# Performance work log

Measured on AMD Instinct MI355X. Metric: run time of the kernel, lower is better.

The kernel has to match this reference:

```python
import jax, jax.numpy as jnp
import numpy as np

SEQ_LEN = 4096
N_FEAT = 2048
N_PADD = 128


def setup_inputs() -> dict:
    key = jax.random.key(0)
    kx, kw = jax.random.split(key)
    x = jax.random.normal(kx, (SEQ_LEN, N_FEAT), dtype=jnp.float32)
    # Fused QKV dense: features = 3 * n_feat
    W = jax.random.normal(kw, (N_FEAT, 3 * N_FEAT), dtype=jnp.float32) * (1.0 / np.sqrt(N_FEAT))
    b = jnp.zeros((3 * N_FEAT,), dtype=jnp.float32)
    return {"x": x, "W": W, "b": b, "n_padd": N_PADD}


def reference(x, W, b, n_padd):
    # Fused QKV projection, split along feature axis (as in nn.Dense + jnp.split)
    qkv = x @ W + b  # [S, 3F]
    q, k, v = jnp.split(qkv, 3, axis=1)  # each [S, F]
    S, F = q.shape
    idx = jnp.arange(S)
    # scores[i, j] = q_i . k_j / sqrt(F)
    scores = (q @ k.T) * (1.0 / jnp.sqrt(jnp.float32(F)))  # [S, S]
    seq_mask = idx >= n_padd                      # valid (non-padding) positions
    causal = idx[None, :] <= idx[:, None]         # j <= i
    mask = causal & seq_mask[None, :]             # kernel: causal_mask & seq_mask
    row_valid = seq_mask                          # rows < n_padd are not computed/stored
    neg_inf = jnp.float32(-jnp.inf)
    scores = jnp.where(mask, scores, neg_inf)
    # Fully-masked (padding) rows would softmax to NaN; neutralize then zero output.
    scores = jnp.where(row_valid[:, None], scores, 0.0)
    att = jax.nn.softmax(scores, axis=-1)         # row-wise stable softmax
    out = att @ v                                 # [S, F]
    out = jnp.where(row_valid[:, None], out, 0.0)  # padded rows produce zeros
    return out
```

## Files before the change

kernel.cpp:

```cpp
#include <hip/hip_runtime.h>
#include <cstdint>
#include <cstddef>
#include <cmath>

typedef unsigned short u16;
typedef short v8s __attribute__((ext_vector_type(8)));
typedef float v4f __attribute__((ext_vector_type(4)));

constexpr int SEQ = 4096;
constexpr int FEAT = 2048;
constexpr int F3 = 6144;


__device__ __forceinline__ u16 f2bf(float f) {
  union { float f; uint32_t u; } v; v.f = f;
  uint32_t r = v.u + 0x7FFFu + ((v.u >> 16) & 1u);
  return (u16)(r >> 16);
}

__device__ __forceinline__ float bf2f(u16 s) {
  union { uint32_t u; float f; } v; v.u = ((uint32_t)s) << 16;
  return v.f;
}

__device__ __forceinline__ void gld_lds16(const u16* g, u16* l) {
  __builtin_amdgcn_global_load_lds(
      (const __attribute__((address_space(1))) void*)g,
      (__attribute__((address_space(3))) void*)l, 16, 0, 0);
}


__global__ void cvt_f32_bf16(const float* __restrict__ in, u16* __restrict__ out, int n8) {
  int i = blockIdx.x * 256 + threadIdx.x;
  if (i >= n8) return;
  const float4* p = (const float4*)in + (size_t)i * 2;
  float4 a = p[0], b = p[1];
  union { u16 s[8]; uint4 v; } u;
  u.s[0] = f2bf(a.x); u.s[1] = f2bf(a.y); u.s[2] = f2bf(a.z); u.s[3] = f2bf(a.w);
  u.s[4] = f2bf(b.x); u.s[5] = f2bf(b.y); u.s[6] = f2bf(b.z); u.s[7] = f2bf(b.w);
  *(uint4*)(out + (size_t)i * 8) = u.v;
}

__global__ void transp_f2b(const float* __restrict__ in, int ldin,
                           u16* __restrict__ out, int ldout) {
  __shared__ float tile[32][33];
  int c0 = blockIdx.x * 32, r0 = blockIdx.y * 32;
  int tx = threadIdx.x, ty = threadIdx.y;
#pragma unroll
  for (int p = 0; p < 4; ++p)
    tile[ty + 8 * p][tx] = in[(size_t)(r0 + ty + 8 * p) * ldin + c0 + tx];
  __syncthreads();
#pragma unroll
  for (int p = 0; p < 4; ++p)
    out[(size_t)(c0 + ty + 8 * p) * ldout + r0 + tx] = f2bf(tile[tx][ty + 8 * p]);
}

__global__ void transp_b2b(const u16* __restrict__ in, int ldin,
                           u16* __restrict__ out, int ldout) {
  __shared__ u16 tile[32][33];
  int c0 = blockIdx.x * 32, r0 = blockIdx.y * 32;
  int tx = threadIdx.x, ty = threadIdx.y;
#pragma unroll
  for (int p = 0; p < 4; ++p)
    tile[ty + 8 * p][tx] = in[(size_t)(r0 + ty + 8 * p) * ldin + c0 + tx];
  __syncthreads();
#pragma unroll
  for (int p = 0; p < 4; ++p)
    out[(size_t)(c0 + ty + 8 * p) * ldout + r0 + tx] = tile[tx][ty + 8 * p];
}


#define BARW() asm volatile("s_barrier" ::: "memory")
#define VMC6() asm volatile("s_waitcnt vmcnt(6)" ::: "memory")

#define STAGE(SB, KO) do { \
  u16* Lb = &LDSU[SB][0] + w * 512; \
  gld_lds16(pA0 + (KO), Lb); \
  gld_lds16(pA0 + (size_t)64 * LDA_ + (KO), Lb + 2048); \
  gld_lds16(pB0 + (KO), Lb + 4096); \
  gld_lds16(pB0 + (size_t)64 * LDB_ + (KO), Lb + 4096 + 2048); \
  gld_lds16(pB0 + (size_t)128 * LDB_ + (KO), Lb + 4096 + 4096); \
  gld_lds16(pB0 + (size_t)192 * LDB_ + (KO), Lb + 4096 + 6144); \
} while (0)

#define LOADA(BUF) do { _Pragma("unroll") \
  for (int mi = 0; mi < 8; ++mi) \
    af[mi] = *(const v8s*)(&LDSU[BUF][0] + (mi * 16 + lm) * 32 + lqs); \
} while (0)

#define LOADB(BUF) do { _Pragma("unroll") \
  for (int ni = 0; ni < 4; ++ni) \
    bf4[ni] = *(const v8s*)(&LDSU[BUF][0] + 4096 + (w * 64 + ni * 16 + lm) * 32 + lqs); \
} while (0)

__device__ __forceinline__ int tri_S(int v) {
  const int u = v >> 1;
  return (v & 1) ? (u + 1) * (u + 1) : u * u + u;
}

template<int LDA_, int LDB_, int LDC_, int OUTMODE ,
         int ADDB, int MODE, int SWZ>
__global__ __launch_bounds__(256, 2) void gemmw(
    const u16* __restrict__ A, const u16* __restrict__ B,
    void* __restrict__ Cv, int K,
    const float* __restrict__ bias, float scale) {
  int bi, bj, ks, ke;
  if (MODE == 2) {
    const int b = blockIdx.x;
    const int cpx = (int)gridDim.x >> 3;
    const int s = (b & 7) * cpx + (b >> 3);
    bi = 2 * (int)sqrtf((float)s);
    while (tri_S(bi + 1) <= s) ++bi;
    while (tri_S(bi) > s) --bi;
    bj = s - tri_S(bi);
    ks = 0; ke = K;
  } else if (MODE == 1) {
    const int f = blockIdx.x;
    bi = ((int)gridDim.x >> 4) - 1 - (f >> 4);
    bj = (f >> 1) & 7;
    const int z = f & 1;
    const int kq = (bi + 1) * 64;
    ks = z ? kq : 0;  ke = ks + kq;
  } else {
    if (SWZ) {
      const int gx = gridDim.x, gy = gridDim.y;
      const int b = blockIdx.y * gx + blockIdx.x;
      const int cpx = (gx * gy) >> 3;
      const int s = (b & 7) * cpx + (b >> 3);
      bi = s % gy;  bj = s / gy;
    } else { bj = blockIdx.x; bi = blockIdx.y; }
    ks = 0; ke = K;
  }
  const int i0 = bi * 128, j0 = bj * 256;

  __shared__ u16 LDSU[3][12288];

  const int t = threadIdx.x;
  const int w = t >> 6, l = t & 63;
  const int lm = l & 15, lq = l >> 4;
  const int lqs = ((lq + (lm >> 1)) & 3) * 8;

  const int l2 = l >> 2;
  const int rA = w * 16 + l2;
  const int cA = ((((l & 3) - ((rA >> 1) & 3)) & 3)) * 8;
  const u16* pA0 = A + (size_t)(i0 + rA) * LDA_ + cA;
  const u16* pB0 = B + (size_t)(j0 + rA) * LDB_ + cA;

  v4f acc[8][4];
#pragma unroll
  for (int a = 0; a < 8; ++a)
#pragma unroll
    for (int b2 = 0; b2 < 4; ++b2)
      acc[a][b2] = v4f{0.f, 0.f, 0.f, 0.f};

  v8s af[8], bf4[4];

  STAGE(0, ks); STAGE(1, ks + 32);
  VMC6(); BARW();
  LOADB(0);

  const int nt = (ke - ks) >> 5;
  int bufr = 0;
  int k2 = ks + 64;
  for (int tt = 0; tt < nt; ++tt) {
    const int sb = (bufr + 2 >= 3) ? bufr - 1 : bufr + 2;
    const int kst = (k2 < ke) ? k2 : ks;
    STAGE(sb, kst);
    LOADA(bufr);
    __builtin_amdgcn_s_setprio(1);
#pragma unroll
    for (int mi = 0; mi < 8; ++mi)
#pragma unroll
      for (int ni = 0; ni < 4; ++ni)
        acc[mi][ni] = __builtin_amdgcn_mfma_f32_16x16x32_bf16(af[mi], bf4[ni], acc[mi][ni], 0, 0, 0);
    __builtin_amdgcn_s_setprio(0);
    VMC6(); BARW();
    const int nb = (bufr == 2) ? 0 : bufr + 1;
    LOADB(nb);
    bufr = nb;
    k2 += 32;
  }

#pragma unroll
  for (int mi = 0; mi < 8; ++mi) {
#pragma unroll
    for (int ni = 0; ni < 4; ++ni) {
      const int cc = j0 + w * 64 + ni * 16 + lm;
      const float badd = ADDB ? bias[cc] : 0.f;
#pragma unroll
      for (int r = 0; r < 4; ++r) {
        const int rr = i0 + mi * 16 + lq * 4 + r;
        if (OUTMODE == 0)
          ((u16*)Cv)[(size_t)rr * LDC_ + cc] = f2bf(acc[mi][ni][r] * scale + badd);
        else
          atomicAdd((float*)Cv + (size_t)rr * LDC_ + cc, acc[mi][ni][r]);
      }
    }
  }
}

__global__ __launch_bounds__(256) void softmax_rows(
    const u16* __restrict__ S0,
    u16* __restrict__ att, const int* __restrict__ npad_p) {
  const int i = blockIdx.x;
  const int np = *npad_p;
  const int kend = ((i >> 7) + 1) << 7;
  const u16* r0 = S0 + (size_t)i * SEQ;
  u16* arow = att + (size_t)i * SEQ;
  const int t = threadIdx.x;

  float m = -3.0e38f, s = 0.f;
  for (int j = np + t; j <= i; j += 256) {
    float v = bf2f(r0[j]);
    if (v > m) { s = s * __expf(m - v) + 1.f; m = v; }
    else       { s += __expf(v - m); }
  }
#pragma unroll
  for (int off = 32; off > 0; off >>= 1) {
    float mo = __shfl_xor(m, off);
    float so = __shfl_xor(s, off);
    float M = fmaxf(m, mo);
    s = s * __expf(m - M) + so * __expf(mo - M);
    m = M;
  }
  __shared__ float sm[4], ss[4];
  const int w = t >> 6, l = t & 63;
  if (l == 0) { sm[w] = m; ss[w] = s; }
  __syncthreads();
  const float M = fmaxf(fmaxf(sm[0], sm[1]), fmaxf(sm[2], sm[3]));
  const float Ssum = ss[0] * __expf(sm[0] - M) + ss[1] * __expf(sm[1] - M) +
                     ss[2] * __expf(sm[2] - M) + ss[3] * __expf(sm[3] - M);
  const float inv = 1.f / Ssum;

  for (int j0b = t * 8; j0b < kend; j0b += 2048) {
    union { u16 s8[8]; uint4 v; } u;
#pragma unroll
    for (int q = 0; q < 8; ++q) {
      const int j = j0b + q;
      float a = 0.f;
      if (j >= np && j <= i)
        a = __expf(bf2f(r0[j]) - M) * inv;
      u.s8[q] = f2bf(a);
    }
    *(uint4*)(arow + j0b) = u.v;
  }
}


extern "C" void kernel_launch(void* const* d_in, const int* in_sizes, int n_in,
                              void* d_out, int out_size, void* d_ws, size_t ws_size,
                              hipStream_t stream) {
  const float* x = (const float*)d_in[0];
  const float* W = (const float*)d_in[1];
  const float* b = (const float*)d_in[2];
  const int* npad = (const int*)d_in[3];
  float* out = (float*)d_out;

  char* p = (char*)d_ws;
  u16* xb = (u16*)p;
  u16* Wt = (u16*)(p + (size_t)SEQ * FEAT * 2);
  u16* att = (u16*)p;
  p += (size_t)SEQ * FEAT * 2 + (size_t)F3 * FEAT * 2;
  u16* qkvb = (u16*)p;  p += (size_t)SEQ * F3 * 2;
  u16* vt   = (u16*)p;  p += (size_t)FEAT * SEQ * 2;
  u16* sc0  = (u16*)p;  p += (size_t)SEQ * SEQ * 2;
  if (ws_size < (size_t)(p - (char*)d_ws)) return;

  const float scale = 0.02209708691207961f;

  hipMemsetAsync(d_out, 0, (size_t)SEQ * FEAT * sizeof(float), stream);

  cvt_f32_bf16<<<SEQ * FEAT / 8 / 256, 256, 0, stream>>>(x, xb, SEQ * FEAT / 8);
  transp_f2b<<<dim3(F3 / 32, FEAT / 32), dim3(32, 8), 0, stream>>>(W, F3, Wt, FEAT);
  gemmw<FEAT, FEAT, F3, 0, 1, 0, 1><<<dim3(F3 / 256, SEQ / 128), 256, 0, stream>>>(
      xb, Wt, (void*)qkvb, FEAT, b, 1.0f);
  transp_b2b<<<dim3(FEAT / 32, SEQ / 32), dim3(32, 8), 0, stream>>>(
      qkvb + 2 * FEAT, F3, vt, SEQ);
  gemmw<F3, F3, SEQ, 0, 0, 2, 0><<<dim3(272), 256, 0, stream>>>(
      qkvb, qkvb + FEAT, (void*)sc0, FEAT, nullptr, scale);
  softmax_rows<<<SEQ, 256, 0, stream>>>(sc0, att, npad);
  gemmw<SEQ, SEQ, FEAT, 1, 0, 1, 0><<<dim3(512), 256, 0, stream>>>(
      att, vt, (void*)out, 0, nullptr, 1.0f);
}
```

Measured before the change: 396.7 us.

## Load GEMM B operand straight into registers and shrink LDS to A only

Each wave read only its own 64-column slice of B from LDS, so the B tile now goes from global memory directly into registers. It is double-buffered in two register sets, and the main loop is unrolled by two to alternate between them. LDS now holds only the triple-buffered A tile, which allows launch bounds of 3 blocks per CU. This removes LDS write and read traffic for B and frees shared memory. In exchange, global-load latency for B sits closer to the MFMA chain, B fetches are less contiguous, and register pressure rises.

```diff
diff --git a/kernel.cpp b/kernel.cpp
--- a/kernel.cpp
+++ b/kernel.cpp
@@ -73,24 +73,29 @@
 #define BARW() asm volatile("s_barrier" ::: "memory")
 #define VMC6() asm volatile("s_waitcnt vmcnt(6)" ::: "memory")
 
-#define STAGE(SB, KO) do { \
-  u16* Lb = &LDSU[SB][0] + w * 512; \
+#define STAGE_A(SB, KO) do { \
+  u16* Lb = &Aldss[SB][0] + w * 512; \
   gld_lds16(pA0 + (KO), Lb); \
   gld_lds16(pA0 + (size_t)64 * LDA_ + (KO), Lb + 2048); \
-  gld_lds16(pB0 + (KO), Lb + 4096); \
-  gld_lds16(pB0 + (size_t)64 * LDB_ + (KO), Lb + 4096 + 2048); \
-  gld_lds16(pB0 + (size_t)128 * LDB_ + (KO), Lb + 4096 + 4096); \
-  gld_lds16(pB0 + (size_t)192 * LDB_ + (KO), Lb + 4096 + 6144); \
 } while (0)
 
 #define LOADA(BUF) do { _Pragma("unroll") \
   for (int mi = 0; mi < 8; ++mi) \
-    af[mi] = *(const v8s*)(&LDSU[BUF][0] + (mi * 16 + lm) * 32 + lqs); \
-} while (0)
-
-#define LOADB(BUF) do { _Pragma("unroll") \
+    af[mi] = *(const v8s*)(&Aldss[BUF][0] + (mi * 16 + lm) * 32 + lqs); \
+} while (0)
+
+#define LOADB_G(DST, KO) do { _Pragma("unroll") \
   for (int ni = 0; ni < 4; ++ni) \
-    bf4[ni] = *(const v8s*)(&LDSU[BUF][0] + 4096 + (w * 64 + ni * 16 + lm) * 32 + lqs); \
+    DST[ni] = *(const v8s*)(pBF + (size_t)(ni * 16) * LDB_ + (KO)); \
+} while (0)
+
+#define MMAW(BF) do { \
+  __builtin_amdgcn_s_setprio(1); \
+  _Pragma("unroll") \
+  for (int mi = 0; mi < 8; ++mi) { _Pragma("unroll") \
+    for (int ni = 0; ni < 4; ++ni) \
+      acc[mi][ni] = __builtin_amdgcn_mfma_f32_16x16x32_bf16(af[mi], BF[ni], acc[mi][ni], 0, 0, 0); } \
+  __builtin_amdgcn_s_setprio(0); \
 } while (0)
 
 __device__ __forceinline__ int tri_S(int v) {
@@ -100,7 +105,7 @@
 
 template<int LDA_, int LDB_, int LDC_, int OUTMODE ,
          int ADDB, int MODE, int SWZ>
-__global__ __launch_bounds__(256, 2) void gemmw(
+__global__ __launch_bounds__(256, 3) void gemmw(
     const u16* __restrict__ A, const u16* __restrict__ B,
     void* __restrict__ Cv, int K,
     const float* __restrict__ bias, float scale) {
@@ -133,18 +138,17 @@
   }
   const int i0 = bi * 128, j0 = bj * 256;
 
-  __shared__ u16 LDSU[3][12288];
+  __shared__ u16 Aldss[3][4096];
 
   const int t = threadIdx.x;
   const int w = t >> 6, l = t & 63;
   const int lm = l & 15, lq = l >> 4;
   const int lqs = ((lq + (lm >> 1)) & 3) * 8;
 
-  const int l2 = l >> 2;
-  const int rA = w * 16 + l2;
+  const int rA = w * 16 + (l >> 2);
   const int cA = ((((l & 3) - ((rA >> 1) & 3)) & 3)) * 8;
   const u16* pA0 = A + (size_t)(i0 + rA) * LDA_ + cA;
-  const u16* pB0 = B + (size_t)(j0 + rA) * LDB_ + cA;
+  const u16* pBF = B + (size_t)(j0 + w * 64 + lm) * LDB_ + lq * 8;
 
   v4f acc[8][4];
 #pragma unroll
@@ -153,32 +157,35 @@
     for (int b2 = 0; b2 < 4; ++b2)
       acc[a][b2] = v4f{0.f, 0.f, 0.f, 0.f};
 
-  v8s af[8], bf4[4];
-
-  STAGE(0, ks); STAGE(1, ks + 32);
+  v8s af[8], bfU[4], bfV[4];
+
+  STAGE_A(0, ks); STAGE_A(1, ks + 32);
+  LOADB_G(bfU, ks);
   VMC6(); BARW();
-  LOADB(0);
 
   const int nt = (ke - ks) >> 5;
-  int bufr = 0;
-  int k2 = ks + 64;
-  for (int tt = 0; tt < nt; ++tt) {
-    const int sb = (bufr + 2 >= 3) ? bufr - 1 : bufr + 2;
-    const int kst = (k2 < ke) ? k2 : ks;
-    STAGE(sb, kst);
-    LOADA(bufr);
-    __builtin_amdgcn_s_setprio(1);
-#pragma unroll
-    for (int mi = 0; mi < 8; ++mi)
-#pragma unroll
-      for (int ni = 0; ni < 4; ++ni)
-        acc[mi][ni] = __builtin_amdgcn_mfma_f32_16x16x32_bf16(af[mi], bf4[ni], acc[mi][ni], 0, 0, 0);
-    __builtin_amdgcn_s_setprio(0);
-    VMC6(); BARW();
-    const int nb = (bufr == 2) ? 0 : bufr + 1;
-    LOADB(nb);
-    bufr = nb;
-    k2 += 32;
+  int b0 = 0, b1 = 1;
+  for (int tt = 0; tt < nt; tt += 2) {
+    const int kc = ks + (tt << 5);
+    const int s2 = 3 - b0 - b1;
+    {
+      const int kst = (kc + 64 < ke) ? kc + 64 : ks;
+      STAGE_A(s2, kst);
+      LOADB_G(bfV, kc + 32);
+      LOADA(b0);
+      MMAW(bfU);
+      VMC6(); BARW();
+    }
+    {
+      const int kst = (kc + 96 < ke) ? kc + 96 : ks;
+      const int kb  = (kc + 64 < ke) ? kc + 64 : ks;
+      STAGE_A(b0, kst);
+      LOADB_G(bfU, kb);
+      LOADA(b1);
+      MMAW(bfV);
+      VMC6(); BARW();
+    }
+    b1 = b0; b0 = s2;
   }
 
 #pragma unroll
```

Result: slower. 1.528 ms (+285.2%).

## Add 256x256 8-wave triangular QK^T GEMM and unroll main gemm loop by two

Applied to the files above, without the earlier changes.

Replaces the 128x256 triangular score GEMM (272 blocks, 4 waves) with a new 256x256 tile kernel using 512 threads (136 blocks). It runs a double-buffered LDS schedule with interleaved half-tile staging and barriers, aiming for higher operand reuse per loaded byte and better overlap of loads with MFMA. The generic gemmw loop is also unrolled by two with explicit buffer rotation, which removes the modulo buffer indexing. Risks include only 136 blocks on a 256-CU part, lower occupancy and heavy barrier use.

```diff
diff --git a/kernel.cpp b/kernel.cpp
--- a/kernel.cpp
+++ b/kernel.cpp
@@ -72,6 +72,7 @@
 
 #define BARW() asm volatile("s_barrier" ::: "memory")
 #define VMC6() asm volatile("s_waitcnt vmcnt(6)" ::: "memory")
+#define LGKM0() asm volatile("s_waitcnt lgkmcnt(0)" ::: "memory")
 
 #define STAGE(SB, KO) do { \
   u16* Lb = &LDSU[SB][0] + w * 512; \
@@ -93,11 +94,6 @@
     bf4[ni] = *(const v8s*)(&LDSU[BUF][0] + 4096 + (w * 64 + ni * 16 + lm) * 32 + lqs); \
 } while (0)
 
-__device__ __forceinline__ int tri_S(int v) {
-  const int u = v >> 1;
-  return (v & 1) ? (u + 1) * (u + 1) : u * u + u;
-}
-
 template<int LDA_, int LDB_, int LDC_, int OUTMODE ,
          int ADDB, int MODE, int SWZ>
 __global__ __launch_bounds__(256, 2) void gemmw(
@@ -105,16 +101,7 @@
     void* __restrict__ Cv, int K,
     const float* __restrict__ bias, float scale) {
   int bi, bj, ks, ke;
-  if (MODE == 2) {
-    const int b = blockIdx.x;
-    const int cpx = (int)gridDim.x >> 3;
-    const int s = (b & 7) * cpx + (b >> 3);
-    bi = 2 * (int)sqrtf((float)s);
-    while (tri_S(bi + 1) <= s) ++bi;
-    while (tri_S(bi) > s) --bi;
-    bj = s - tri_S(bi);
-    ks = 0; ke = K;
-  } else if (MODE == 1) {
+  if (MODE == 1) {
     const int f = blockIdx.x;
     bi = ((int)gridDim.x >> 4) - 1 - (f >> 4);
     bj = (f >> 1) & 7;
@@ -140,8 +127,7 @@
   const int lm = l & 15, lq = l >> 4;
   const int lqs = ((lq + (lm >> 1)) & 3) * 8;
 
-  const int l2 = l >> 2;
-  const int rA = w * 16 + l2;
+  const int rA = w * 16 + (l >> 2);
   const int cA = ((((l & 3) - ((rA >> 1) & 3)) & 3)) * 8;
   const u16* pA0 = A + (size_t)(i0 + rA) * LDA_ + cA;
   const u16* pB0 = B + (size_t)(j0 + rA) * LDB_ + cA;
@@ -160,25 +146,39 @@
   LOADB(0);
 
   const int nt = (ke - ks) >> 5;
-  int bufr = 0;
-  int k2 = ks + 64;
-  for (int tt = 0; tt < nt; ++tt) {
-    const int sb = (bufr + 2 >= 3) ? bufr - 1 : bufr + 2;
-    const int kst = (k2 < ke) ? k2 : ks;
-    STAGE(sb, kst);
-    LOADA(bufr);
-    __builtin_amdgcn_s_setprio(1);
-#pragma unroll
-    for (int mi = 0; mi < 8; ++mi)
-#pragma unroll
-      for (int ni = 0; ni < 4; ++ni)
-        acc[mi][ni] = __builtin_amdgcn_mfma_f32_16x16x32_bf16(af[mi], bf4[ni], acc[mi][ni], 0, 0, 0);
-    __builtin_amdgcn_s_setprio(0);
-    VMC6(); BARW();
-    const int nb = (bufr == 2) ? 0 : bufr + 1;
-    LOADB(nb);
-    bufr = nb;
-    k2 += 32;
+  int b0 = 0, b1 = 1;
+  for (int tt = 0; tt < nt; tt += 2) {
+    const int kc = ks + (tt << 5);
+    const int s2 = 3 - b0 - b1;
+    {
+      const int kst = (kc + 64 < ke) ? kc + 64 : ks;
+      STAGE(s2, kst);
+      LOADA(b0);
+      __builtin_amdgcn_s_setprio(1);
+#pragma unroll
+      for (int mi = 0; mi < 8; ++mi)
+#pragma unroll
+        for (int ni = 0; ni < 4; ++ni)
+          acc[mi][ni] = __builtin_amdgcn_mfma_f32_16x16x32_bf16(af[mi], bf4[ni], acc[mi][ni], 0, 0, 0);
+      __builtin_amdgcn_s_setprio(0);
+      VMC6(); BARW();
+      LOADB(b1);
+    }
+    {
+      const int kst = (kc + 96 < ke) ? kc + 96 : ks;
+      STAGE(b0, kst);
+      LOADA(b1);
+      __builtin_amdgcn_s_setprio(1);
+#pragma unroll
+      for (int mi = 0; mi < 8; ++mi)
+#pragma unroll
+        for (int ni = 0; ni < 4; ++ni)
+          acc[mi][ni] = __builtin_amdgcn_mfma_f32_16x16x32_bf16(af[mi], bf4[ni], acc[mi][ni], 0, 0, 0);
+      __builtin_amdgcn_s_setprio(0);
+      VMC6(); BARW();
+      LOADB(s2);
+    }
+    b1 = b0; b0 = s2;
   }
 
 #pragma unroll
@@ -198,6 +198,152 @@
     }
   }
 }
+
+#undef STAGE
+#undef LOADA
+#undef LOADB
+
+
+#define LDA8(BUF, MH) do { _Pragma("unroll") \
+  for (int fi = 0; fi < 4; ++fi) { \
+    const u16* ap = &As8[BUF][wr][(MH) * 4096 + fi * 1024]; \
+    af[fi][0] = *(const v8s*)(ap + off0); \
+    af[fi][1] = *(const v8s*)(ap + off1); \
+  } } while (0)
+
+#define LDB8(BUF) do { _Pragma("unroll") \
+  for (int ni = 0; ni < 4; ++ni) { \
+    const u16* bp = &Bs8[BUF][bh][bo + ni * 1024]; \
+    bfr[ni][0] = *(const v8s*)(bp + off0); \
+    bfr[ni][1] = *(const v8s*)(bp + off1); \
+  } } while (0)
+
+#define MMA8(MH, NL) do { _Pragma("unroll") \
+  for (int fi = 0; fi < 4; ++fi) { _Pragma("unroll") \
+    for (int nn = 0; nn < 2; ++nn) { \
+      acc[(MH)*4+fi][(NL)+nn] = __builtin_amdgcn_mfma_f32_16x16x32_bf16( \
+          af[fi][0], bfr[(NL)+nn][0], acc[(MH)*4+fi][(NL)+nn], 0, 0, 0); \
+      acc[(MH)*4+fi][(NL)+nn] = __builtin_amdgcn_mfma_f32_16x16x32_bf16( \
+          af[fi][1], bfr[(NL)+nn][1], acc[(MH)*4+fi][(NL)+nn], 0, 0, 0); \
+    } } } while (0)
+
+#define STG8A(BUF, H, KO) do { \
+  gld_lds16(Ag + (size_t)(H) * 128 * LDA_ + (KO), &As8[BUF][H][w8 * 1024]); \
+  gld_lds16(Ag + ((size_t)(H) * 128 + 8) * LDA_ + (KO), &As8[BUF][H][w8 * 1024 + 512]); \
+  } while (0)
+
+#define STG8B(BUF, H, KO) do { \
+  gld_lds16(Bg + (size_t)(H) * 128 * LDB_ + (KO), &Bs8[BUF][H][w8 * 1024]); \
+  gld_lds16(Bg + ((size_t)(H) * 128 + 8) * LDB_ + (KO), &Bs8[BUF][H][w8 * 1024 + 512]); \
+  } while (0)
+
+template<int LDA_, int LDB_, int LDC_>
+__global__ __launch_bounds__(512, 2) void gemm8tri(
+    const u16* __restrict__ A, const u16* __restrict__ B,
+    u16* __restrict__ C, int K, float scale) {
+  const int b = blockIdx.x;
+  const int cpx = (int)gridDim.x >> 3;
+  const int s = (b & 7) * cpx + (b >> 3);
+  int bi = (int)((sqrtf(8.f * s + 1.f) - 1.f) * 0.5f);
+  while ((bi + 1) * (bi + 2) / 2 <= s) ++bi;
+  while (bi * (bi + 1) / 2 > s) --bi;
+  const int bj = s - bi * (bi + 1) / 2;
+  const int i0 = bi * 256, j0 = bj * 256;
+
+  __shared__ u16 As8[2][2][8192];
+  __shared__ u16 Bs8[2][2][8192];
+
+  const int t = threadIdx.x;
+  const int w8 = t >> 6, l = t & 63;
+  const int wr = w8 >> 2, wc = w8 & 3;
+  const int lm = l & 15, lq = l >> 4;
+  const int bh = wc >> 1, bo = (wc & 1) * 4096;
+
+  const int off0 = lm * 64 + ((lq + lm) & 7) * 8;
+  const int off1 = lm * 64 + ((lq + lm + 4) & 7) * 8;
+
+  const int srow = w8 * 16 + (l >> 3);
+  const int scol = (((l & 7) - (l >> 3)) & 7) * 8;
+  const u16* Ag = A + (size_t)(i0 + srow) * LDA_ + scol;
+  const u16* Bg = B + (size_t)(j0 + srow) * LDB_ + scol;
+
+  v4f acc[8][4];
+#pragma unroll
+  for (int a = 0; a < 8; ++a)
+#pragma unroll
+    for (int b2 = 0; b2 < 4; ++b2)
+      acc[a][b2] = v4f{0.f, 0.f, 0.f, 0.f};
+
+  v8s af[4][2], bfr[4][2];
+
+  STG8B(0, 0, 0); STG8B(0, 1, 0); STG8A(0, 0, 0); STG8A(0, 1, 0);
+  STG8B(1, 0, 64); STG8B(1, 1, 64); STG8A(1, 0, 64);
+  VMC6(); BARW();
+
+  const int nit = K >> 7;
+  for (int it = 0; it < nit; ++it) {
+    const int kc = it << 7;
+    const int k1 = kc + 64;
+    int k2 = kc + 128; if (k2 >= K) k2 = 0;
+    int k3 = kc + 192; if (k3 >= K) k3 = 0;
+
+    LDA8(0, 0); LDB8(0);
+    STG8A(1, 1, k1);
+    BARW(); LGKM0();
+    __builtin_amdgcn_s_setprio(1); MMA8(0, 0); __builtin_amdgcn_s_setprio(0);
+    BARW();
+    STG8B(0, 0, k2);
+    BARW();
+    __builtin_amdgcn_s_setprio(1); MMA8(0, 2); __builtin_amdgcn_s_setprio(0);
+    BARW();
+    LDA8(0, 1);
+    STG8B(0, 1, k2);
+    BARW(); LGKM0();
+    __builtin_amdgcn_s_setprio(1); MMA8(1, 0); __builtin_amdgcn_s_setprio(0);
+    BARW();
+    STG8A(0, 0, k2);
+    BARW();
+    __builtin_amdgcn_s_setprio(1); MMA8(1, 2); __builtin_amdgcn_s_setprio(0);
+    VMC6(); BARW();
+    LDA8(1, 0); LDB8(1);
+    STG8A(0, 1, k2);
+    BARW(); LGKM0();
+    __builtin_amdgcn_s_setprio(1); MMA8(0, 0); __builtin_amdgcn_s_setprio(0);
+    BARW();
+    STG8B(1, 0, k3);
+    BARW();
+    __builtin_amdgcn_s_setprio(1); MMA8(0, 2); __builtin_amdgcn_s_setprio(0);
+    BARW();
+    LDA8(1, 1);
+    STG8B(1, 1, k3);
+    BARW(); LGKM0();
+    __builtin_amdgcn_s_setprio(1); MMA8(1, 0); __builtin_amdgcn_s_setprio(0);
+    BARW();
+    STG8A(1, 0, k3);
+    BARW();
+    __builtin_amdgcn_s_setprio(1); MMA8(1, 2); __builtin_amdgcn_s_setprio(0);
+    VMC6(); BARW();
+  }
+
+#pragma unroll
+  for (int mi = 0; mi < 8; ++mi) {
+#pragma unroll
+    for (int ni = 0; ni < 4; ++ni) {
+      const int cc = j0 + wc * 64 + ni * 16 + lm;
+#pragma unroll
+      for (int r = 0; r < 4; ++r) {
+        const int rr = i0 + wr * 128 + mi * 16 + lq * 4 + r;
+        C[(size_t)rr * LDC_ + cc] = f2bf(acc[mi][ni][r] * scale);
+      }
+    }
+  }
+}
+
+#undef LDA8
+#undef LDB8
+#undef MMA8
+#undef STG8A
+#undef STG8B
 
 __global__ __launch_bounds__(256) void softmax_rows(
     const u16* __restrict__ S0,
@@ -276,8 +422,8 @@
       xb, Wt, (void*)qkvb, FEAT, b, 1.0f);
   transp_b2b<<<dim3(FEAT / 32, SEQ / 32), dim3(32, 8), 0, stream>>>(
       qkvb + 2 * FEAT, F3, vt, SEQ);
-  gemmw<F3, F3, SEQ, 0, 0, 2, 0><<<dim3(272), 256, 0, stream>>>(
-      qkvb, qkvb + FEAT, (void*)sc0, FEAT, nullptr, scale);
+  gemm8tri<F3, F3, SEQ><<<dim3(136), 512, 0, stream>>>(
+      qkvb, qkvb + FEAT, sc0, FEAT, scale);
   softmax_rows<<<SEQ, 256, 0, stream>>>(sc0, att, npad);
   gemmw<SEQ, SEQ, FEAT, 1, 0, 1, 0><<<dim3(512), 256, 0, stream>>>(
       att, vt, (void*)out, 0, nullptr, 1.0f);
```

Result: no change. 393.2 us (-0.9%).
